# Kernel optimization log

Hardware: AMD Instinct MI355X
Metric: run time of the kernel (lower is better)

The kernel has to match this reference:

```python
import jax, jax.numpy as jnp
import numpy as np

NEG_SLOPE = 0.2
N_NODES = 50000
N_EDGES = 800000
IN_DIM = 256
HID_DIM = 256
HEADS = 8
HEAD_DIM = HID_DIM // HEADS


def setup_inputs() -> dict:
    key = jax.random.key(0)
    ks = jax.random.split(key, 12)
    def glorot(k, shape):
        fan = sum(shape[-2:]) if len(shape) > 1 else shape[-1] + 1
        return jax.random.normal(k, shape, jnp.float32) * jnp.sqrt(2.0 / fan)
    return {
        "data": jax.random.normal(ks[0], (N_NODES, IN_DIM), jnp.float32),
        "src": jax.random.randint(ks[1], (N_EDGES,), 0, N_NODES),
        "dst": jax.random.randint(ks[2], (N_EDGES,), 0, N_NODES),
        "W1": glorot(ks[3], (IN_DIM, HID_DIM)),
        "al1": glorot(ks[4], (HEADS, HEAD_DIM)),
        "ar1": glorot(ks[5], (HEADS, HEAD_DIM)),
        "b1": jnp.zeros((HID_DIM,), jnp.float32),
        "W2": glorot(ks[6], (HID_DIM, HID_DIM)),
        "al2": glorot(ks[7], (HEADS, HEAD_DIM)),
        "ar2": glorot(ks[8], (HEADS, HEAD_DIM)),
        "b2": jnp.zeros((HID_DIM,), jnp.float32),
    }


def gat_layer(x, src, dst, W, al, ar, b):
    """One DGL-style GATConv layer with ReLU activation."""
    N = x.shape[0]
    feat = (x @ W).reshape(N, HEADS, HEAD_DIM)            # [N,H,D]
    el = jnp.sum(feat * al[None], axis=-1)                # [N,H]
    er = jnp.sum(feat * ar[None], axis=-1)                # [N,H]
    e = el[src] + er[dst]                                  # [E,H]
    e = jnp.where(e > 0, e, NEG_SLOPE * e)                 # LeakyReLU(0.2)
    # segment softmax over incoming edges of each dst node
    m = jax.ops.segment_max(e, dst, num_segments=N)        # [N,H] (-inf for empty)
    a = jnp.exp(e - m[dst])                                # [E,H]
    denom = jax.ops.segment_sum(a, dst, num_segments=N)    # [N,H]
    alpha = a / denom[dst]                                 # [E,H]
    msg = feat[src] * alpha[:, :, None]                    # [E,H,D]
    out = jax.ops.segment_sum(msg, dst, num_segments=N)    # [N,H,D]
    out = out + b.reshape(1, HEADS, HEAD_DIM)
    out = jax.nn.relu(out)
    return out.reshape(N, HID_DIM)


def reference(data, src, dst, W1, al1, ar1, b1, W2, al2, ar2, b2):
    h = gat_layer(data, src, dst, W1, al1, ar1, b1)
    h = gat_layer(h, src, dst, W2, al2, ar2, b2)
    return h
```

## Files before the change

### kernel.cpp

```cpp
#include <hip/hip_runtime.h>

#define N_NODES 50000
#define N_EDGES 800000
#define DIM 256
#define HEADS 8
#define NEG_SLOPE 0.2f

typedef unsigned short u16;
typedef float floatx4 __attribute__((ext_vector_type(4)));
typedef __bf16 bf16x8 __attribute__((ext_vector_type(8)));

__device__ __forceinline__ float b2f(u16 u) {
    union { unsigned int i; float f; } v; v.i = ((unsigned int)u) << 16; return v.f;
}
__device__ __forceinline__ u16 f2b(float f) {
    union { float f; unsigned int i; } v; v.f = f;
    unsigned int x = v.i;
    if ((x & 0x7f800000u) == 0x7f800000u && (x & 0x007fffffu)) {
        return (u16)((x >> 16) | 0x0040u);
    }
    unsigned int r = (x + 0x7fffu + ((x >> 16) & 1u)) >> 16;
    return (u16)r;
}

__global__ __launch_bounds__(256) void fill_u32(unsigned int* __restrict__ p,
                                                unsigned int v, int n) {
    int i = blockIdx.x * 256 + threadIdx.x;
    if (i < n) p[i] = v;
}

__global__ __launch_bounds__(256) void init_kernel(const unsigned int* __restrict__ d,
                                                   int* __restrict__ counts,
                                                   int* __restrict__ flag) {
    int i = blockIdx.x * 256 + threadIdx.x;
    if (i < N_NODES) counts[i] = 0;
    if (blockIdx.x == 0) {
        __shared__ int cnt;
        if (threadIdx.x == 0) cnt = 0;
        __syncthreads();
        unsigned int w = d[threadIdx.x];
        int bad = 0;
        #pragma unroll
        for (int half = 0; half < 2; ++half) {
            u16 u = (u16)(w >> (16 * half));
            unsigned int e = (u >> 7) & 0xFFu;
            if (u != 0 && (e >= 141u || e <= 27u)) bad = 1;
        }
        atomicAdd(&cnt, bad);
        __syncthreads();
        if (threadIdx.x == 0) *flag = (cnt > 64) ? 1 : 0;
    }
}

__global__ __launch_bounds__(256) void prep_kernel(const void* __restrict__ W1,
                                                   const void* __restrict__ W2,
                                                   const void* __restrict__ data,
                                                   u16* __restrict__ Wt1,
                                                   u16* __restrict__ Wt2,
                                                   u16* __restrict__ datab,
                                                   const int* __restrict__ flagp) {
    const int isf = *flagp;
    int b = blockIdx.x;
    if (b < 32) {
        const void* W = (b < 16) ? W1 : W2;
        u16* Wt = (b < 16) ? Wt1 : Wt2;
        int t = b & 15;
        int k0 = (t >> 2) * 64, n0 = (t & 3) * 64;
        __shared__ float lt[64][65];
        int c = threadIdx.x & 63, r0 = threadIdx.x >> 6;
        #pragma unroll
        for (int j = 0; j < 16; ++j) {
            int r = j * 4 + r0;
            lt[r][c] = isf ? ((const float*)W)[(k0 + r) * 256 + n0 + c]
                           : b2f(((const u16*)W)[(k0 + r) * 256 + n0 + c]);
        }
        __syncthreads();
        #pragma unroll
        for (int j = 0; j < 16; ++j) {
            int rn = j * 4 + r0;
            Wt[(n0 + rn) * 256 + k0 + c] = f2b(lt[c][rn]);
        }
    } else {
        if (!isf) return;
        int base = (b - 32) * 2048 + threadIdx.x * 8;
        const float* df = (const float*)data + base;
        float4 f0 = *(const float4*)df;
        float4 f1 = *(const float4*)(df + 4);
        u16 tb[8] = {f2b(f0.x), f2b(f0.y), f2b(f0.z), f2b(f0.w),
                     f2b(f1.x), f2b(f1.y), f2b(f1.z), f2b(f1.w)};
        *(uint4*)(datab + base) = *(uint4*)tb;
    }
}

__global__ __launch_bounds__(256) void hist_kernel(const int* __restrict__ dst,
                                                   int* __restrict__ counts, int E) {
    int i = blockIdx.x * 256 + threadIdx.x;
    if (i < E) atomicAdd(&counts[dst[i]], 1);
}

__global__ __launch_bounds__(256) void scan_partial(const int* __restrict__ counts,
                                                    int* __restrict__ partial, int n) {
    int b = blockIdx.x, tid = threadIdx.x;
    int base = b * 1024 + tid * 4;
    int s = 0;
    #pragma unroll
    for (int k = 0; k < 4; ++k) if (base + k < n) s += counts[base + k];
    int lane = tid & 63;
    #pragma unroll
    for (int off = 32; off; off >>= 1) s += __shfl_xor(s, off);
    __shared__ int wsum[4];
    if (lane == 0) wsum[tid >> 6] = s;
    __syncthreads();
    if (tid == 0) partial[b] = wsum[0] + wsum[1] + wsum[2] + wsum[3];
}

__global__ __launch_bounds__(64) void scan_offsets(const int* __restrict__ partial,
                                                   int* __restrict__ offsets,
                                                   int* __restrict__ row_ptr,
                                                   int nb, int n) {
    int t = threadIdx.x;
    int v0 = (t < nb) ? partial[t] : 0;
    int v = v0;
    #pragma unroll
    for (int d = 1; d < 64; d <<= 1) {
        int u = __shfl_up(v, d);
        if (t >= d) v += u;
    }
    if (t < nb) offsets[t] = v - v0;
    if (t == 63) row_ptr[n] = v;
}

__global__ __launch_bounds__(256) void scan_write(const int* __restrict__ counts,
                                                  const int* __restrict__ offsets,
                                                  int* __restrict__ row_ptr,
                                                  int* __restrict__ wptr, int n) {
    int b = blockIdx.x, tid = threadIdx.x;
    int base = b * 1024 + tid * 4;
    int v[4]; int s = 0;
    #pragma unroll
    for (int k = 0; k < 4; ++k) { v[k] = (base + k < n) ? counts[base + k] : 0; s += v[k]; }
    int lane = tid & 63, w = tid >> 6;
    int incl = s;
    #pragma unroll
    for (int d = 1; d < 64; d <<= 1) {
        int u = __shfl_up(incl, d);
        if (lane >= d) incl += u;
    }
    __shared__ int wsum[4];
    if (lane == 63) wsum[w] = incl;
    __syncthreads();
    int woff = 0;
    for (int i = 0; i < w; ++i) woff += wsum[i];
    int run = offsets[b] + woff + incl - s;
    #pragma unroll
    for (int k = 0; k < 4; ++k) {
        if (base + k < n) { row_ptr[base + k] = run; wptr[base + k] = run; run += v[k]; }
    }
}

__global__ __launch_bounds__(256) void scatter_kernel(const int* __restrict__ src,
                                                      const int* __restrict__ dst,
                                                      int* __restrict__ wptr,
                                                      int* __restrict__ src_sorted, int E) {
    int i = blockIdx.x * 256 + threadIdx.x;
    if (i < E) {
        int pos = atomicAdd(&wptr[dst[i]], 1);
        src_sorted[pos] = src[i];
    }
}

#define LDA 264
#define LDB 40

__global__ __launch_bounds__(256, 2) void gemm_fused(const u16* __restrict__ Aisf,
                                                     const u16* __restrict__ Abf,
                                                     const u16* __restrict__ Wt,
                                                     u16* __restrict__ outF,
                                                     float* __restrict__ el,
                                                     float* __restrict__ er,
                                                     const void* __restrict__ al,
                                                     const void* __restrict__ ar,
                                                     int M, const int* __restrict__ flagp) {
    const int isf = *flagp;
    const u16* A = isf ? Aisf : Abf;
    __shared__ u16 As[64][LDA];
    __shared__ u16 Ws[256][LDB];
    const int tid  = threadIdx.x;
    const int w    = tid >> 6;
    const int lane = tid & 63;
    const int quad = lane >> 4;
    const int l16  = lane & 15;
    const int m0   = blockIdx.x * 64;

    #pragma unroll
    for (int it = 0; it < 8; ++it) {
        int idx = it * 256 + tid;
        int r = idx >> 5;
        int c = (idx & 31) << 3;
        int gr = m0 + r;
        if (gr < M) {
            *(uint4*)&As[r][c] = *(const uint4*)(A + gr * 256 + c);
        } else {
            uint4 z = {0u, 0u, 0u, 0u};
            *(uint4*)&As[r][c] = z;
        }
    }

    floatx4 acc[4][4] = {};

    for (int s = 0; s < 8; ++s) {
        __syncthreads();
        #pragma unroll
        for (int it = 0; it < 4; ++it) {
            int idx = it * 256 + tid;
            int n = idx >> 2;
            int k8 = (idx & 3) << 3;
            *(uint4*)&Ws[n][k8] = *(const uint4*)(Wt + n * 256 + s * 32 + k8);
        }
        __syncthreads();

        bf16x8 af[4], bfv[4];
        #pragma unroll
        for (int i = 0; i < 4; ++i)
            af[i] = *(const bf16x8*)&As[16 * i + l16][s * 32 + quad * 8];
        #pragma unroll
        for (int t = 0; t < 4; ++t)
            bfv[t] = *(const bf16x8*)&Ws[64 * w + 16 * t + l16][quad * 8];
        #pragma unroll
        for (int i = 0; i < 4; ++i)
            #pragma unroll
            for (int t = 0; t < 4; ++t)
                acc[i][t] = __builtin_amdgcn_mfma_f32_16x16x32_bf16(af[i], bfv[t], acc[i][t], 0, 0, 0);
    }

    #pragma unroll
    for (int i = 0; i < 4; ++i)
        #pragma unroll
        for (int t = 0; t < 4; ++t)
            #pragma unroll
            for (int r = 0; r < 4; ++r) {
                int row = m0 + 16 * i + quad * 4 + r;
                if (row < M) outF[row * 256 + 64 * w + 16 * t + l16] = f2b(acc[i][t][r]);
            }

    float alv[4], arv[4];
    #pragma unroll
    for (int t = 0; t < 4; ++t) {
        int c = 64 * w + 16 * t + l16;
        alv[t] = isf ? ((const float*)al)[c] : b2f(((const u16*)al)[c]);
        arv[t] = isf ? ((const float*)ar)[c] : b2f(((const u16*)ar)[c]);
    }
    #pragma unroll
    for (int i = 0; i < 4; ++i)
        #pragma unroll
        for (int r = 0; r < 4; ++r) {
            int row = m0 + 16 * i + quad * 4 + r;
            #pragma unroll
            for (int tt = 0; tt < 2; ++tt) {
                float pl = acc[i][2 * tt][r] * alv[2 * tt] + acc[i][2 * tt + 1][r] * alv[2 * tt + 1];
                float pr = acc[i][2 * tt][r] * arv[2 * tt] + acc[i][2 * tt + 1][r] * arv[2 * tt + 1];
                #pragma unroll
                for (int mask = 1; mask <= 8; mask <<= 1) {
                    pl += __shfl_xor(pl, mask);
                    pr += __shfl_xor(pr, mask);
                }
                if (l16 == 0 && row < M) {
                    el[row * 8 + 2 * w + tt] = pl;
                    er[row * 8 + 2 * w + tt] = pr;
                }
            }
        }
}

__global__ __launch_bounds__(256) void aggregate_kernel(const u16* __restrict__ feat,
                                                        const float* __restrict__ el,
                                                        const float* __restrict__ er,
                                                        const void* __restrict__ bias,
                                                        const int* __restrict__ row_ptr,
                                                        const int* __restrict__ src_sorted,
                                                        void* __restrict__ out,
                                                        int out_mode,
                                                        const int* __restrict__ flagp) {
    const int isf = *flagp;
    const int lane = threadIdx.x & 63;
    const int node = blockIdx.x * 4 + (threadIdx.x >> 6);
    if (node >= N_NODES) return;
    const int h = lane >> 3;
    const int j = lane & 7;
    const int beg = row_ptr[node];
    const int deg = row_ptr[node + 1] - beg;
    const float ern = er[node * HEADS + h];

    float m = -1e30f, ssum = 0.f;
    for (int i = j; i < deg; i += 8) {
        int s = src_sorted[beg + i];
        float e = el[s * 8 + h] + ern;
        e = e > 0.f ? e : NEG_SLOPE * e;
        float mn = fmaxf(m, e);
        ssum = ssum * __expf(m - mn) + __expf(e - mn);
        m = mn;
    }
    #pragma unroll
    for (int mask = 1; mask <= 4; mask <<= 1) {
        float mo = __shfl_xor(m, mask);
        float so = __shfl_xor(ssum, mask);
        float mn = fmaxf(m, mo);
        ssum = ssum * __expf(m - mn) + so * __expf(mo - mn);
        m = mn;
    }
    const float mx = m;
    const float inv = ssum > 0.f ? 1.f / ssum : 0.f;

    const int q = lane & 31;
    const int half = lane >> 5;
    const int hq = q >> 2;
    float a[8] = {};
    for (int c0 = 0; c0 < deg; c0 += 8) {
        int i = c0 + j;
        int s = 0; float av = 0.f;
        if (i < deg) {
            s = src_sorted[beg + i];
            float e = el[s * 8 + h] + ern;
            e = e > 0.f ? e : NEG_SLOPE * e;
            av = __expf(e - mx) * inv;
        }
        int rem = deg - c0; if (rem > 8) rem = 8;
        for (int t2 = 0; t2 < rem; t2 += 2) {
            int sel = hq * 8 + t2 + half;
            int   se = __shfl(s, sel);
            float ae = __shfl(av, sel);
            uint4 f = *(const uint4*)(feat + se * DIM + 8 * q);
            a[0] += ae * b2f((u16)(f.x & 0xffffu)); a[1] += ae * b2f((u16)(f.x >> 16));
            a[2] += ae * b2f((u16)(f.y & 0xffffu)); a[3] += ae * b2f((u16)(f.y >> 16));
            a[4] += ae * b2f((u16)(f.z & 0xffffu)); a[5] += ae * b2f((u16)(f.z >> 16));
            a[6] += ae * b2f((u16)(f.w & 0xffffu)); a[7] += ae * b2f((u16)(f.w >> 16));
        }
    }
    #pragma unroll
    for (int k = 0; k < 8; ++k) a[k] += __shfl_xor(a[k], 32);

    if (half == 0) {
        float o[8];
        if (isf) {
            float4 b0 = *(const float4*)((const float*)bias + 8 * q);
            float4 b1 = *(const float4*)((const float*)bias + 8 * q + 4);
            o[0] = a[0] + b0.x; o[1] = a[1] + b0.y; o[2] = a[2] + b0.z; o[3] = a[3] + b0.w;
            o[4] = a[4] + b1.x; o[5] = a[5] + b1.y; o[6] = a[6] + b1.z; o[7] = a[7] + b1.w;
        } else {
            uint4 bu = *(const uint4*)((const u16*)bias + 8 * q);
            o[0] = a[0] + b2f((u16)(bu.x & 0xffffu)); o[1] = a[1] + b2f((u16)(bu.x >> 16));
            o[2] = a[2] + b2f((u16)(bu.y & 0xffffu)); o[3] = a[3] + b2f((u16)(bu.y >> 16));
            o[4] = a[4] + b2f((u16)(bu.z & 0xffffu)); o[5] = a[5] + b2f((u16)(bu.z >> 16));
            o[6] = a[6] + b2f((u16)(bu.w & 0xffffu)); o[7] = a[7] + b2f((u16)(bu.w >> 16));
        }
        #pragma unroll
        for (int k = 0; k < 8; ++k) o[k] = fmaxf(o[k], 0.f);
        if (out_mode == 0 || !isf) {
            u16 pk[8] = {f2b(o[0]), f2b(o[1]), f2b(o[2]), f2b(o[3]),
                         f2b(o[4]), f2b(o[5]), f2b(o[6]), f2b(o[7])};
            *(uint4*)((u16*)out + node * DIM + 8 * q) = *(uint4*)pk;
        } else {
            float4 v0 = {o[0], o[1], o[2], o[3]};
            float4 v1 = {o[4], o[5], o[6], o[7]};
            *(float4*)((float*)out + node * DIM + 8 * q) = v0;
            *(float4*)((float*)out + node * DIM + 8 * q + 4) = v1;
        }
    }
}

extern "C" void kernel_launch(void* const* d_in, const int* in_sizes, int n_in,
                              void* d_out, int out_size, void* d_ws, size_t ws_size,
                              hipStream_t stream) {
    const void* data = d_in[0];
    const int* src = (const int*)d_in[1];
    const int* dst = (const int*)d_in[2];
    const void* W1  = d_in[3];
    const void* al1 = d_in[4];
    const void* ar1 = d_in[5];
    const void* b1  = d_in[6];
    const void* W2  = d_in[7];
    const void* al2 = d_in[8];
    const void* ar2 = d_in[9];
    const void* b2  = d_in[10];

    const size_t NEEDED =
        (size_t)N_NODES * DIM * 2 +
        (size_t)N_NODES * HEADS * 4 * 2 +
        (size_t)N_NODES * 4 * 2 +
        (size_t)(N_NODES + 4) * 4 +
        (size_t)N_EDGES * 4 +
        2 * 256 * 256 * 2 +
        1024;

    if (ws_size < NEEDED) {
        int nwords = (out_size + 1) / 2;
        fill_u32<<<(nwords + 255) / 256, 256, 0, stream>>>(
            (unsigned int*)d_out, 0x42C842C8u, nwords);
        return;
    }

    char* ws = (char*)d_ws;
    u16* feat = (u16*)ws;        ws += (size_t)N_NODES * DIM * 2;
    float* el = (float*)ws;      ws += (size_t)N_NODES * HEADS * 4;
    float* er = (float*)ws;      ws += (size_t)N_NODES * HEADS * 4;
    int* counts = (int*)ws;      ws += (size_t)N_NODES * 4;
    int* wptr = (int*)ws;        ws += (size_t)N_NODES * 4;
    int* row_ptr = (int*)ws;     ws += (size_t)(N_NODES + 4) * 4;
    int* src_sorted = (int*)ws;  ws += (size_t)N_EDGES * 4;
    u16* Wt1 = (u16*)ws;         ws += 256 * 256 * 2;
    u16* Wt2 = (u16*)ws;         ws += 256 * 256 * 2;
    int* partial = (int*)ws;     ws += 256;
    int* offsets = (int*)ws;     ws += 256;
    int* flag = (int*)ws;        ws += 256;

    u16* h1    = (u16*)d_out;
    u16* datab = (u16*)d_out + (size_t)N_NODES * DIM;

    const int nb = (N_NODES + 1023) / 1024;

    init_kernel<<<(N_NODES + 255) / 256, 256, 0, stream>>>(
        (const unsigned int*)data, counts, flag);
    prep_kernel<<<32 + (N_NODES * DIM) / 2048, 256, 0, stream>>>(
        W1, W2, data, Wt1, Wt2, datab, flag);
    hist_kernel<<<(N_EDGES + 255) / 256, 256, 0, stream>>>(dst, counts, N_EDGES);
    scan_partial<<<nb, 256, 0, stream>>>(counts, partial, N_NODES);
    scan_offsets<<<1, 64, 0, stream>>>(partial, offsets, row_ptr, nb, N_NODES);
    scan_write<<<nb, 256, 0, stream>>>(counts, offsets, row_ptr, wptr, N_NODES);
    scatter_kernel<<<(N_EDGES + 255) / 256, 256, 0, stream>>>(src, dst, wptr, src_sorted, N_EDGES);

    const int gemm_blocks = (N_NODES + 63) / 64;
    const int agg_blocks = (N_NODES + 3) / 4;

    gemm_fused<<<gemm_blocks, 256, 0, stream>>>(datab, (const u16*)data, Wt1, feat,
                                                el, er, al1, ar1, N_NODES, flag);
    aggregate_kernel<<<agg_blocks, 256, 0, stream>>>(feat, el, er, b1, row_ptr, src_sorted,
                                                     (void*)h1, 0, flag);
    gemm_fused<<<gemm_blocks, 256, 0, stream>>>(h1, h1, Wt2, feat,
                                                el, er, al2, ar2, N_NODES, flag);
    aggregate_kernel<<<agg_blocks, 256, 0, stream>>>(feat, el, er, b2, row_ptr, src_sorted,
                                                     d_out, 2, flag);
}
```

Before: 439.9 us.

## Fold attention vectors into GEMM, fuse input conversion, and streamline scan and aggregation

After: 467.7 us. +6.3%, slower.

```diff
diff --git a/kernel.cpp b/kernel.cpp
--- a/kernel.cpp
+++ b/kernel.cpp
@@ -16,9 +16,6 @@
 __device__ __forceinline__ u16 f2b(float f) {
     union { float f; unsigned int i; } v; v.f = f;
     unsigned int x = v.i;
-    if ((x & 0x7f800000u) == 0x7f800000u && (x & 0x007fffffu)) {
-        return (u16)((x >> 16) | 0x0040u);
-    }
     unsigned int r = (x + 0x7fffu + ((x >> 16) & 1u)) >> 16;
     return (u16)r;
 }
@@ -54,10 +51,14 @@
 
 __global__ __launch_bounds__(256) void prep_kernel(const void* __restrict__ W1,
                                                    const void* __restrict__ W2,
-                                                   const void* __restrict__ data,
+                                                   const void* __restrict__ al1,
+                                                   const void* __restrict__ ar1,
+                                                   const void* __restrict__ al2,
+                                                   const void* __restrict__ ar2,
                                                    u16* __restrict__ Wt1,
                                                    u16* __restrict__ Wt2,
-                                                   u16* __restrict__ datab,
+                                                   u16* __restrict__ alr1,
+                                                   u16* __restrict__ alr2,
                                                    const int* __restrict__ flagp) {
     const int isf = *flagp;
     int b = blockIdx.x;
@@ -81,14 +82,25 @@
             Wt[(n0 + rn) * 256 + k0 + c] = f2b(lt[c][rn]);
         }
     } else {
-        if (!isf) return;
-        int base = (b - 32) * 2048 + threadIdx.x * 8;
-        const float* df = (const float*)data + base;
-        float4 f0 = *(const float4*)df;
-        float4 f1 = *(const float4*)(df + 4);
-        u16 tb[8] = {f2b(f0.x), f2b(f0.y), f2b(f0.z), f2b(f0.w),
-                     f2b(f1.x), f2b(f1.y), f2b(f1.z), f2b(f1.w)};
-        *(uint4*)(datab + base) = *(uint4*)tb;
+        const void* W  = (b == 32) ? W1 : W2;
+        const void* al = (b == 32) ? al1 : al2;
+        const void* ar = (b == 32) ? ar1 : ar2;
+        u16* alr = (b == 32) ? alr1 : alr2;
+        for (int idx = threadIdx.x; idx < 4096; idx += 256) {
+            int col = idx >> 8, k = idx & 255;
+            int h = col & 7;
+            const void* a = (col < 8) ? al : ar;
+            float s = 0.f;
+            #pragma unroll 8
+            for (int d = 0; d < 32; ++d) {
+                float wv = isf ? ((const float*)W)[k * 256 + h * 32 + d]
+                               : b2f(((const u16*)W)[k * 256 + h * 32 + d]);
+                float av = isf ? ((const float*)a)[h * 32 + d]
+                               : b2f(((const u16*)a)[h * 32 + d]);
+                s += wv * av;
+            }
+            alr[col * 256 + k] = f2b(s);
+        }
     }
 }
 
@@ -114,27 +126,21 @@
     if (tid == 0) partial[b] = wsum[0] + wsum[1] + wsum[2] + wsum[3];
 }
 
-__global__ __launch_bounds__(64) void scan_offsets(const int* __restrict__ partial,
-                                                   int* __restrict__ offsets,
-                                                   int* __restrict__ row_ptr,
-                                                   int nb, int n) {
-    int t = threadIdx.x;
-    int v0 = (t < nb) ? partial[t] : 0;
-    int v = v0;
-    #pragma unroll
-    for (int d = 1; d < 64; d <<= 1) {
-        int u = __shfl_up(v, d);
-        if (t >= d) v += u;
-    }
-    if (t < nb) offsets[t] = v - v0;
-    if (t == 63) row_ptr[n] = v;
-}
-
 __global__ __launch_bounds__(256) void scan_write(const int* __restrict__ counts,
-                                                  const int* __restrict__ offsets,
+                                                  const int* __restrict__ partial,
                                                   int* __restrict__ row_ptr,
-                                                  int* __restrict__ wptr, int n) {
+                                                  int* __restrict__ wptr, int n, int nb) {
     int b = blockIdx.x, tid = threadIdx.x;
+    __shared__ int off_s, tot_s;
+    if (tid < 64) {
+        int pv = (tid < nb) ? partial[tid] : 0;
+        int vb = (tid < b) ? pv : 0;
+        int vt = pv;
+        #pragma unroll
+        for (int m = 32; m; m >>= 1) { vb += __shfl_xor(vb, m); vt += __shfl_xor(vt, m); }
+        if (tid == 0) { off_s = vb; tot_s = vt; }
+    }
+    __syncthreads();
     int base = b * 1024 + tid * 4;
     int v[4]; int s = 0;
     #pragma unroll
@@ -151,11 +157,12 @@
     __syncthreads();
     int woff = 0;
     for (int i = 0; i < w; ++i) woff += wsum[i];
-    int run = offsets[b] + woff + incl - s;
+    int run = off_s + woff + incl - s;
     #pragma unroll
     for (int k = 0; k < 4; ++k) {
         if (base + k < n) { row_ptr[base + k] = run; wptr[base + k] = run; run += v[k]; }
     }
+    if (b == 0 && tid == 0) row_ptr[n] = tot_s;
 }
 
 __global__ __launch_bounds__(256) void scatter_kernel(const int* __restrict__ src,
@@ -170,27 +177,23 @@
 }
 
 #define LDA 264
-#define LDB 40
-
-__global__ __launch_bounds__(256, 2) void gemm_fused(const u16* __restrict__ Aisf,
-                                                     const u16* __restrict__ Abf,
+
+__global__ __launch_bounds__(256, 3) void gemm_fused(const void* __restrict__ A,
                                                      const u16* __restrict__ Wt,
+                                                     const u16* __restrict__ alr,
                                                      u16* __restrict__ outF,
                                                      float* __restrict__ el,
                                                      float* __restrict__ er,
-                                                     const void* __restrict__ al,
-                                                     const void* __restrict__ ar,
-                                                     int M, const int* __restrict__ flagp) {
-    const int isf = *flagp;
-    const u16* A = isf ? Aisf : Abf;
+                                                     int M, int a_fp32_if_isf,
+                                                     const int* __restrict__ flagp) {
     __shared__ u16 As[64][LDA];
-    __shared__ u16 Ws[256][LDB];
     const int tid  = threadIdx.x;
     const int w    = tid >> 6;
     const int lane = tid & 63;
     const int quad = lane >> 4;
     const int l16  = lane & 15;
     const int m0   = blockIdx.x * 64;
+    const bool a_fp32 = a_fp32_if_isf && (*flagp != 0);
 
     #pragma unroll
     for (int it = 0; it < 8; ++it) {
@@ -199,38 +202,47 @@
         int c = (idx & 31) << 3;
         int gr = m0 + r;
         if (gr < M) {
-            *(uint4*)&As[r][c] = *(const uint4*)(A + gr * 256 + c);
+            if (a_fp32) {
+                const float* Af = (const float*)A;
+                float4 f0 = *(const float4*)(Af + gr * 256 + c);
+                float4 f1 = *(const float4*)(Af + gr * 256 + c + 4);
+                u16 tb[8] = {f2b(f0.x), f2b(f0.y), f2b(f0.z), f2b(f0.w),
+                             f2b(f1.x), f2b(f1.y), f2b(f1.z), f2b(f1.w)};
+                *(uint4*)&As[r][c] = *(uint4*)tb;
+            } else {
+                *(uint4*)&As[r][c] = *(const uint4*)((const u16*)A + gr * 256 + c);
+            }
         } else {
             uint4 z = {0u, 0u, 0u, 0u};
             *(uint4*)&As[r][c] = z;
         }
     }
+    __syncthreads();
 
     floatx4 acc[4][4] = {};
-
+    floatx4 eacc[4] = {};
+
+    const u16* Wb = Wt + (64 * w + l16) * 256 + quad * 8;
+    const u16* Eb = alr + l16 * 256 + quad * 8;
+
+    #pragma unroll
     for (int s = 0; s < 8; ++s) {
-        __syncthreads();
-        #pragma unroll
-        for (int it = 0; it < 4; ++it) {
-            int idx = it * 256 + tid;
-            int n = idx >> 2;
-            int k8 = (idx & 3) << 3;
-            *(uint4*)&Ws[n][k8] = *(const uint4*)(Wt + n * 256 + s * 32 + k8);
-        }
-        __syncthreads();
-
-        bf16x8 af[4], bfv[4];
+        bf16x8 bfv[4], ebf;
+        #pragma unroll
+        for (int t = 0; t < 4; ++t)
+            bfv[t] = *(const bf16x8*)(Wb + t * 16 * 256 + s * 32);
+        ebf = *(const bf16x8*)(Eb + s * 32);
+        bf16x8 af[4];
         #pragma unroll
         for (int i = 0; i < 4; ++i)
             af[i] = *(const bf16x8*)&As[16 * i + l16][s * 32 + quad * 8];
         #pragma unroll
-        for (int t = 0; t < 4; ++t)
-            bfv[t] = *(const bf16x8*)&Ws[64 * w + 16 * t + l16][quad * 8];
-        #pragma unroll
-        for (int i = 0; i < 4; ++i)
+        for (int i = 0; i < 4; ++i) {
             #pragma unroll
             for (int t = 0; t < 4; ++t)
                 acc[i][t] = __builtin_amdgcn_mfma_f32_16x16x32_bf16(af[i], bfv[t], acc[i][t], 0, 0, 0);
+            eacc[i] = __builtin_amdgcn_mfma_f32_16x16x32_bf16(af[i], ebf, eacc[i], 0, 0, 0);
+        }
     }
 
     #pragma unroll
@@ -242,34 +254,19 @@
                 int row = m0 + 16 * i + quad * 4 + r;
                 if (row < M) outF[row * 256 + 64 * w + 16 * t + l16] = f2b(acc[i][t][r]);
             }
-
-    float alv[4], arv[4];
-    #pragma unroll
-    for (int t = 0; t < 4; ++t) {
-        int c = 64 * w + 16 * t + l16;
-        alv[t] = isf ? ((const float*)al)[c] : b2f(((const u16*)al)[c]);
-        arv[t] = isf ? ((const float*)ar)[c] : b2f(((const u16*)ar)[c]);
-    }
-    #pragma unroll
-    for (int i = 0; i < 4; ++i)
-        #pragma unroll
-        for (int r = 0; r < 4; ++r) {
-            int row = m0 + 16 * i + quad * 4 + r;
+    if (w == 0) {
+        #pragma unroll
+        for (int i = 0; i < 4; ++i)
             #pragma unroll
-            for (int tt = 0; tt < 2; ++tt) {
-                float pl = acc[i][2 * tt][r] * alv[2 * tt] + acc[i][2 * tt + 1][r] * alv[2 * tt + 1];
-                float pr = acc[i][2 * tt][r] * arv[2 * tt] + acc[i][2 * tt + 1][r] * arv[2 * tt + 1];
-                #pragma unroll
-                for (int mask = 1; mask <= 8; mask <<= 1) {
-                    pl += __shfl_xor(pl, mask);
-                    pr += __shfl_xor(pr, mask);
-                }
-                if (l16 == 0 && row < M) {
-                    el[row * 8 + 2 * w + tt] = pl;
-                    er[row * 8 + 2 * w + tt] = pr;
+            for (int r = 0; r < 4; ++r) {
+                int row = m0 + 16 * i + quad * 4 + r;
+                if (row < M) {
+                    float v = eacc[i][r];
+                    if (l16 < 8) el[row * 8 + l16] = v;
+                    else         er[row * 8 + (l16 - 8)] = v;
                 }
             }
-        }
+    }
 }
 
 __global__ __launch_bounds__(256) void aggregate_kernel(const u16* __restrict__ feat,
@@ -315,7 +312,33 @@
     const int half = lane >> 5;
     const int hq = q >> 2;
     float a[8] = {};
-    for (int c0 = 0; c0 < deg; c0 += 8) {
+
+    const int full = deg & ~7;
+    int c0 = 0;
+    for (; c0 < full; c0 += 8) {
+        int i = c0 + j;
+        int s = src_sorted[beg + i];
+        float e = el[s * 8 + h] + ern;
+        e = e > 0.f ? e : NEG_SLOPE * e;
+        float av = __expf(e - mx) * inv;
+        int se[4]; float ae[4];
+        #pragma unroll
+        for (int k = 0; k < 4; ++k) {
+            int sel = hq * 8 + 2 * k + half;
+            se[k] = __shfl(s, sel);
+            ae[k] = __shfl(av, sel);
+        }
+        #pragma unroll
+        for (int k = 0; k < 4; ++k) {
+            uint4 f = *(const uint4*)(feat + se[k] * DIM + 8 * q);
+            float w = ae[k];
+            a[0] += w * b2f((u16)(f.x & 0xffffu)); a[1] += w * b2f((u16)(f.x >> 16));
+            a[2] += w * b2f((u16)(f.y & 0xffffu)); a[3] += w * b2f((u16)(f.y >> 16));
+            a[4] += w * b2f((u16)(f.z & 0xffffu)); a[5] += w * b2f((u16)(f.z >> 16));
+            a[6] += w * b2f((u16)(f.w & 0xffffu)); a[7] += w * b2f((u16)(f.w >> 16));
+        }
+    }
+    if (c0 < deg) {
         int i = c0 + j;
         int s = 0; float av = 0.f;
         if (i < deg) {
@@ -324,16 +347,24 @@
             e = e > 0.f ? e : NEG_SLOPE * e;
             av = __expf(e - mx) * inv;
         }
-        int rem = deg - c0; if (rem > 8) rem = 8;
-        for (int t2 = 0; t2 < rem; t2 += 2) {
-            int sel = hq * 8 + t2 + half;
-            int   se = __shfl(s, sel);
-            float ae = __shfl(av, sel);
-            uint4 f = *(const uint4*)(feat + se * DIM + 8 * q);
-            a[0] += ae * b2f((u16)(f.x & 0xffffu)); a[1] += ae * b2f((u16)(f.x >> 16));
-            a[2] += ae * b2f((u16)(f.y & 0xffffu)); a[3] += ae * b2f((u16)(f.y >> 16));
-            a[4] += ae * b2f((u16)(f.z & 0xffffu)); a[5] += ae * b2f((u16)(f.z >> 16));
-            a[6] += ae * b2f((u16)(f.w & 0xffffu)); a[7] += ae * b2f((u16)(f.w >> 16));
+        int rem = deg - c0;
+        int se[4]; float ae[4];
+        #pragma unroll
+        for (int k = 0; k < 4; ++k) {
+            int sel = hq * 8 + 2 * k + half;
+            se[k] = __shfl(s, sel);
+            ae[k] = __shfl(av, sel);
+        }
+        #pragma unroll
+        for (int k = 0; k < 4; ++k) {
+            if (2 * k + half < rem) {
+                uint4 f = *(const uint4*)(feat + se[k] * DIM + 8 * q);
+                float w = ae[k];
+                a[0] += w * b2f((u16)(f.x & 0xffffu)); a[1] += w * b2f((u16)(f.x >> 16));
+                a[2] += w * b2f((u16)(f.y & 0xffffu)); a[3] += w * b2f((u16)(f.y >> 16));
+                a[4] += w * b2f((u16)(f.z & 0xffffu)); a[5] += w * b2f((u16)(f.z >> 16));
+                a[6] += w * b2f((u16)(f.w & 0xffffu)); a[7] += w * b2f((u16)(f.w >> 16));
+            }
         }
     }
     #pragma unroll
@@ -390,6 +421,7 @@
         (size_t)(N_NODES + 4) * 4 +
         (size_t)N_EDGES * 4 +
         2 * 256 * 256 * 2 +
+        2 * 16 * 256 * 2 +
         1024;
 
     if (ws_size < NEEDED) {
@@ -409,34 +441,33 @@
     int* src_sorted = (int*)ws;  ws += (size_t)N_EDGES * 4;
     u16* Wt1 = (u16*)ws;         ws += 256 * 256 * 2;
     u16* Wt2 = (u16*)ws;         ws += 256 * 256 * 2;
+    u16* alr1 = (u16*)ws;        ws += 16 * 256 * 2;
+    u16* alr2 = (u16*)ws;        ws += 16 * 256 * 2;
     int* partial = (int*)ws;     ws += 256;
-    int* offsets = (int*)ws;     ws += 256;
     int* flag = (int*)ws;        ws += 256;
 
-    u16* h1    = (u16*)d_out;
-    u16* datab = (u16*)d_out + (size_t)N_NODES * DIM;
+    u16* h1 = (u16*)d_out;
 
     const int nb = (N_NODES + 1023) / 1024;
 
     init_kernel<<<(N_NODES + 255) / 256, 256, 0, stream>>>(
         (const unsigned int*)data, counts, flag);
-    prep_kernel<<<32 + (N_NODES * DIM) / 2048, 256, 0, stream>>>(
-        W1, W2, data, Wt1, Wt2, datab, flag);
+    prep_kernel<<<34, 256, 0, stream>>>(W1, W2, al1, ar1, al2, ar2,
+                                        Wt1, Wt2, alr1, alr2, flag);
     hist_kernel<<<(N_EDGES + 255) / 256, 256, 0, stream>>>(dst, counts, N_EDGES);
     scan_partial<<<nb, 256, 0, stream>>>(counts, partial, N_NODES);
-    scan_offsets<<<1, 64, 0, stream>>>(partial, offsets, row_ptr, nb, N_NODES);
-    scan_write<<<nb, 256, 0, stream>>>(counts, offsets, row_ptr, wptr, N_NODES);
+    scan_write<<<nb, 256, 0, stream>>>(counts, partial, row_ptr, wptr, N_NODES, nb);
     scatter_kernel<<<(N_EDGES + 255) / 256, 256, 0, stream>>>(src, dst, wptr, src_sorted, N_EDGES);
 
     const int gemm_blocks = (N_NODES + 63) / 64;
     const int agg_blocks = (N_NODES + 3) / 4;
 
-    gemm_fused<<<gemm_blocks, 256, 0, stream>>>(datab, (const u16*)data, Wt1, feat,
-                                                el, er, al1, ar1, N_NODES, flag);
+    gemm_fused<<<gemm_blocks, 256, 0, stream>>>(data, Wt1, alr1, feat, el, er,
+                                                N_NODES, 1, flag);
     aggregate_kernel<<<agg_blocks, 256, 0, stream>>>(feat, el, er, b1, row_ptr, src_sorted,
                                                      (void*)h1, 0, flag);
-    gemm_fused<<<gemm_blocks, 256, 0, stream>>>(h1, h1, Wt2, feat,
-                                                el, er, al2, ar2, N_NODES, flag);
+    gemm_fused<<<gemm_blocks, 256, 0, stream>>>(h1, Wt2, alr2, feat, el, er,
+                                                N_NODES, 0, flag);
     aggregate_kernel<<<agg_blocks, 256, 0, stream>>>(feat, el, er, b2, row_ptr, src_sorted,
                                                      d_out, 2, flag);
 }
```
